# Performance work log

Hardware: AMD Instinct MI355X
Metric: run time of the kernel (lower is better)

## Reference

```python
import jax, jax.numpy as jnp
import numpy as np

LAMBDA = 0.5
TAU = 1.0
EPS = 1e-8  # torch F.cosine_similarity eps

B, D = 8192, 1024


def setup_inputs() -> dict:
    key = jax.random.key(0)
    k1, k2, k3, k4 = jax.random.split(key, 4)
    return {
        "student_query_emb": jax.random.normal(k1, (B, D), dtype=jnp.float32),
        "student_passage_emb": jax.random.normal(k2, (B, D), dtype=jnp.float32),
        "teacher_query_emb": jax.random.normal(k3, (B, D), dtype=jnp.float32),
        "teacher_passage_emb": jax.random.normal(k4, (B, D), dtype=jnp.float32),
    }


def _mse(a, b):
    d = a - b
    return jnp.mean(d * d)


def _retrieval_loss(q, p):
    # cosine sim = (q . p) / max(||q|| * ||p||, eps); normalize then matmul
    # (avoids the [B,B,D] broadcast intermediate of the torch version)
    qn = q / jnp.maximum(jnp.linalg.norm(q, axis=-1, keepdims=True), EPS)
    pn = p / jnp.maximum(jnp.linalg.norm(p, axis=-1, keepdims=True), EPS)
    logits = jnp.einsum("bd,cd->bc", qn, pn) / TAU  # [B, B]
    # cross-entropy with labels = arange(B): pick the diagonal log-prob
    logprobs = jax.nn.log_softmax(logits, axis=-1)
    return -jnp.mean(jnp.diagonal(logprobs))


def reference(student_query_emb, student_passage_emb, teacher_query_emb, teacher_passage_emb):
    distill = 0.5 * (_mse(student_query_emb, teacher_query_emb)
                     + _mse(student_passage_emb, teacher_passage_emb))
    retrieval = _retrieval_loss(student_query_emb, student_passage_emb)
    return LAMBDA * distill + (1.0 - LAMBDA) * retrieval
```

## Files before the change

kernel.cpp:

```cpp
#include <hip/hip_runtime.h>
#include <hip/hip_bf16.h>

typedef unsigned short u16;
typedef unsigned char u8;
typedef float f32x4 __attribute__((ext_vector_type(4)));
typedef int int4v __attribute__((ext_vector_type(4)));
typedef int int8v __attribute__((ext_vector_type(8)));

#define B_ROWS 8192
#define D_DIM  1024
#define FP8_SCALE 16.0f
#define ACC_UNSCALE (1.0f/256.0f)


__global__ void __launch_bounds__(256) prep_kernel(
    const float* __restrict__ sq, const float* __restrict__ sp,
    const float* __restrict__ tq, const float* __restrict__ tp,
    int* __restrict__ qn, int* __restrict__ pn,
    float* __restrict__ ppq, float* __restrict__ ppp, float* __restrict__ ppd)
{
    const int wave = threadIdx.x >> 6;
    const int l    = threadIdx.x & 63;
    const int r    = blockIdx.x * 4 + wave;
    const size_t rb4 = (size_t)r * (D_DIM / 4);

    const float4* Q4 = (const float4*)sq + rb4;
    const float4* P4 = (const float4*)sp + rb4;
    const float4* A4 = (const float4*)tq + rb4;
    const float4* B4 = (const float4*)tp + rb4;

    float4 qv[4], pv[4];
    float sq2 = 0.f, sp2 = 0.f, dq = 0.f, dp = 0.f, qp = 0.f;
    #pragma unroll
    for (int j = 0; j < 4; ++j) {
        const int idx = j * 64 + l;
        float4 q = Q4[idx], p = P4[idx], a = A4[idx], b = B4[idx];
        qv[j] = q; pv[j] = p;
        sq2 += q.x*q.x + q.y*q.y + q.z*q.z + q.w*q.w;
        sp2 += p.x*p.x + p.y*p.y + p.z*p.z + p.w*p.w;
        float dx = q.x-a.x, dy = q.y-a.y, dz = q.z-a.z, dw = q.w-a.w;
        dq += dx*dx + dy*dy + dz*dz + dw*dw;
        dx = p.x-b.x; dy = p.y-b.y; dz = p.z-b.z; dw = p.w-b.w;
        dp += dx*dx + dy*dy + dz*dz + dw*dw;
        qp += q.x*p.x + q.y*p.y + q.z*p.z + q.w*p.w;
    }

    #pragma unroll
    for (int m = 1; m <= 32; m <<= 1) {
        sq2 += __shfl_xor(sq2, m);
        sp2 += __shfl_xor(sp2, m);
        dq  += __shfl_xor(dq, m);
        dp  += __shfl_xor(dp, m);
        qp  += __shfl_xor(qp, m);
    }

    const float rq = 1.0f / fmaxf(sqrtf(sq2), 1e-8f);
    const float rp = 1.0f / fmaxf(sqrtf(sp2), 1e-8f);

    if (l == 0) {
        ppq[r] = dq;
        ppp[r] = dp;
        ppd[r] = qp * rq * rp;
    }

    const float fq = rq * FP8_SCALE;
    const float fp = rp * FP8_SCALE;
    int* qrow = qn + (size_t)r * (D_DIM / 4);
    int* prow = pn + (size_t)r * (D_DIM / 4);
    #pragma unroll
    for (int j = 0; j < 4; ++j) {
        const int idx = j * 64 + l;
        int pk = __builtin_amdgcn_cvt_pk_fp8_f32(qv[j].x * fq, qv[j].y * fq, 0, false);
        pk     = __builtin_amdgcn_cvt_pk_fp8_f32(qv[j].z * fq, qv[j].w * fq, pk, true);
        qrow[idx] = pk;
        pk = __builtin_amdgcn_cvt_pk_fp8_f32(pv[j].x * fp, pv[j].y * fp, 0, false);
        pk = __builtin_amdgcn_cvt_pk_fp8_f32(pv[j].z * fp, pv[j].w * fp, pk, true);
        prow[idx] = pk;
    }
}

union Frag { int8v v8; struct { int4v lo, hi; } h; };

__global__ void __launch_bounds__(512, 2) gemm_rowsum_kernel(
    const u8* __restrict__ Q, const u8* __restrict__ P,
    float* __restrict__ gpart)
{
    __shared__ u8 smA[2][256 * 128];
    __shared__ u8 smB[2][256 * 128];

    const int tid  = threadIdx.x;
    const int wave = tid >> 6;
    const int lane = tid & 63;
    const int wm   = wave >> 2;
    const int wn   = wave & 3;
    const int bm   = blockIdx.y;
    const int bn   = blockIdx.x;

    const int srow   = tid >> 3;
    const int schunk = (tid & 7) ^ (srow & 7);
    const u8* Ag = Q + (size_t)(bm * 256 + srow) * D_DIM + schunk * 16;
    const u8* Bg = P + (size_t)(bn * 256 + srow) * D_DIM + schunk * 16;
    const int ldsw = wave * 1024;

#define STAGE_A(b, rbase, k0)                                                  \
    __builtin_amdgcn_global_load_lds(                                          \
        (const __attribute__((address_space(1))) void*)(Ag + (size_t)(rbase) * D_DIM + (k0)), \
        (__attribute__((address_space(3))) void*)(&smA[b][(rbase) * 128] + ldsw), 16, 0, 0)
#define STAGE_B(b, rbase, k0)                                                  \
    __builtin_amdgcn_global_load_lds(                                          \
        (const __attribute__((address_space(1))) void*)(Bg + (size_t)(rbase) * D_DIM + (k0)), \
        (__attribute__((address_space(3))) void*)(&smB[b][(rbase) * 128] + ldsw), 16, 0, 0)

    const int quad = lane >> 4;
    const int rw   = lane & 15;
    const int r7   = lane & 7;
    const int off_lo = ((2 * quad) ^ r7) * 16;
    const int off_hi = ((2 * quad + 1) ^ r7) * 16;
    const int arow_base = (wm * 128 + rw) * 128;
    const int brow_base = (wn * 64  + rw) * 128;

    f32x4 acc[8][4];
    #pragma unroll
    for (int i = 0; i < 8; ++i)
        #pragma unroll
        for (int j = 0; j < 4; ++j)
            acc[i][j] = (f32x4){0.f, 0.f, 0.f, 0.f};

    STAGE_A(0, 0, 0);   STAGE_A(0, 64, 0);   STAGE_A(0, 128, 0);   STAGE_A(0, 192, 0);
    STAGE_B(0, 0, 0);   STAGE_B(0, 64, 0);   STAGE_B(0, 128, 0);   STAGE_B(0, 192, 0);
    STAGE_A(1, 0, 128); STAGE_A(1, 64, 128); STAGE_A(1, 128, 128); STAGE_A(1, 192, 128);
    STAGE_B(1, 0, 128); STAGE_B(1, 64, 128);

#define MFMA_QUAD(mih, nih)                                                    \
    _Pragma("unroll")                                                          \
    for (int mi = 0; mi < 4; ++mi)                                             \
      _Pragma("unroll")                                                        \
      for (int ni = 0; ni < 2; ++ni)                                           \
        acc[(mih)*4 + mi][(nih)*2 + ni] =                                      \
            __builtin_amdgcn_mfma_scale_f32_16x16x128_f8f6f4(                  \
                af[(mih)*4 + mi].v8, bf[(nih)*2 + ni].v8,                      \
                acc[(mih)*4 + mi][(nih)*2 + ni],                               \
                0, 0, 0, 0x7f7f7f7f, 0, 0x7f7f7f7f);

#define KSTEP(t, DO_B1, DO_T2, VMN)                                            \
  {                                                                            \
    constexpr int cur = (t) & 1;                                               \
    if (DO_B1) { STAGE_B(cur ^ 1, 128, ((t) + 1) * 128);                       \
                 STAGE_B(cur ^ 1, 192, ((t) + 1) * 128); }                     \
    asm volatile("s_waitcnt vmcnt(" #VMN ")" ::: "memory");                    \
    __builtin_amdgcn_s_barrier();                                              \
    __builtin_amdgcn_sched_barrier(0);                                         \
    Frag af[8], bf[4];                                                         \
    const u8* sA_ = &smA[cur][0];                                              \
    const u8* sB_ = &smB[cur][0];                                              \
    _Pragma("unroll")                                                          \
    for (int mi = 0; mi < 8; ++mi)                                             \
      af[mi].h.lo = *(const int4v*)(sA_ + arow_base + mi * 2048 + off_lo);     \
    _Pragma("unroll")                                                          \
    for (int ni = 0; ni < 4; ++ni)                                             \
      bf[ni].h.lo = *(const int4v*)(sB_ + brow_base + ni * 2048 + off_lo);     \
    __builtin_amdgcn_sched_barrier(0);                                         \
    _Pragma("unroll")                                                          \
    for (int mi = 0; mi < 8; ++mi)                                             \
      af[mi].h.hi = *(const int4v*)(sA_ + arow_base + mi * 2048 + off_hi);     \
    _Pragma("unroll")                                                          \
    for (int ni = 0; ni < 4; ++ni)                                             \
      bf[ni].h.hi = *(const int4v*)(sB_ + brow_base + ni * 2048 + off_hi);     \
    asm volatile("s_waitcnt lgkmcnt(0)" ::: "memory");                         \
    __builtin_amdgcn_sched_barrier(0);                                         \
    __builtin_amdgcn_s_barrier();                                              \
    __builtin_amdgcn_s_setprio(1); MFMA_QUAD(0, 0) __builtin_amdgcn_s_setprio(0); \
    if (DO_T2) { STAGE_A(cur, 0,   ((t) + 2) * 128); STAGE_A(cur, 64,  ((t) + 2) * 128); } \
    __builtin_amdgcn_s_setprio(1); MFMA_QUAD(0, 1) __builtin_amdgcn_s_setprio(0); \
    if (DO_T2) { STAGE_A(cur, 128, ((t) + 2) * 128); STAGE_A(cur, 192, ((t) + 2) * 128); } \
    __builtin_amdgcn_s_setprio(1); MFMA_QUAD(1, 0) __builtin_amdgcn_s_setprio(0); \
    if (DO_T2) { STAGE_B(cur, 0,   ((t) + 2) * 128); STAGE_B(cur, 64,  ((t) + 2) * 128); } \
    __builtin_amdgcn_s_setprio(1); MFMA_QUAD(1, 1) __builtin_amdgcn_s_setprio(0); \
  }

    KSTEP(0, true,  true,  8)
    KSTEP(1, true,  true,  8)
    KSTEP(2, true,  true,  8)
    KSTEP(3, true,  true,  8)
    KSTEP(4, true,  true,  8)
    KSTEP(5, true,  true,  8)
    KSTEP(6, true,  false, 8)
    KSTEP(7, false, false, 0)

#undef KSTEP
#undef MFMA_QUAD
#undef STAGE_A
#undef STAGE_B

    float esum[8][4];
    #pragma unroll
    for (int mi = 0; mi < 8; ++mi)
        #pragma unroll
        for (int r = 0; r < 4; ++r) {
            float s = 0.f;
            #pragma unroll
            for (int ni = 0; ni < 4; ++ni)
                s += __expf(acc[mi][ni][r] * ACC_UNSCALE);
            esum[mi][r] = s;
        }
    #pragma unroll
    for (int m = 1; m <= 8; m <<= 1)
        #pragma unroll
        for (int mi = 0; mi < 8; ++mi)
            #pragma unroll
            for (int r = 0; r < 4; ++r)
                esum[mi][r] += __shfl_xor(esum[mi][r], m);

    if (rw == 0) {
        float* dst = gpart + (size_t)(bn * 4 + wn) * B_ROWS
                   + bm * 256 + wm * 128;
        #pragma unroll
        for (int mi = 0; mi < 8; ++mi)
            #pragma unroll
            for (int r = 0; r < 4; ++r)
                dst[mi * 16 + quad * 4 + r] = esum[mi][r];
    }
}

__global__ void __launch_bounds__(256) reduce_kernel(
    const float* __restrict__ gpart,
    const float* __restrict__ ppq, const float* __restrict__ ppp,
    const float* __restrict__ ppd, float4* __restrict__ bpart)
{
    const int t = threadIdx.x;
    const int r = blockIdx.x * 256 + t;
    float s = 0.f;
    #pragma unroll 8
    for (int j = 0; j < 128; ++j) s += gpart[(size_t)j * B_ROWS + r];
    float ls = logf(s);
    float v2 = ppq[r], v3 = ppp[r], v4 = ppd[r];
    #pragma unroll
    for (int m = 1; m <= 32; m <<= 1) {
        ls += __shfl_xor(ls, m);
        v2 += __shfl_xor(v2, m);
        v3 += __shfl_xor(v3, m);
        v4 += __shfl_xor(v4, m);
    }
    __shared__ float red[4][4];
    if ((t & 63) == 0) {
        red[t >> 6][0] = ls; red[t >> 6][1] = v2;
        red[t >> 6][2] = v3; red[t >> 6][3] = v4;
    }
    __syncthreads();
    if (t == 0) {
        float4 o;
        o.x = red[0][0] + red[1][0] + red[2][0] + red[3][0];
        o.y = red[0][1] + red[1][1] + red[2][1] + red[3][1];
        o.z = red[0][2] + red[1][2] + red[2][2] + red[3][2];
        o.w = red[0][3] + red[1][3] + red[2][3] + red[3][3];
        bpart[blockIdx.x] = o;
    }
}

__global__ void __launch_bounds__(64) finalize_kernel(
    const float4* __restrict__ bpart, float* __restrict__ out)
{
    const int t = threadIdx.x;
    float4 v = (t < 32) ? bpart[t] : (float4){0.f, 0.f, 0.f, 0.f};
    #pragma unroll
    for (int m = 1; m <= 16; m <<= 1) {
        v.x += __shfl_xor(v.x, m);
        v.y += __shfl_xor(v.y, m);
        v.z += __shfl_xor(v.z, m);
        v.w += __shfl_xor(v.w, m);
    }
    if (t == 0) {
        const float inv_bd = 1.0f / ((float)B_ROWS * (float)D_DIM);
        float distill   = 0.5f * (v.y + v.z) * inv_bd;
        float retrieval = (v.x - v.w) / (float)B_ROWS;
        out[0] = 0.5f * distill + 0.5f * retrieval;
    }
}

extern "C" void kernel_launch(void* const* d_in, const int* in_sizes, int n_in,
                              void* d_out, int out_size, void* d_ws, size_t ws_size,
                              hipStream_t stream) {
    const float* sq = (const float*)d_in[0];
    const float* sp = (const float*)d_in[1];
    const float* tq = (const float*)d_in[2];
    const float* tp = (const float*)d_in[3];

    char* ws = (char*)d_ws;
    float*  ppq   = (float*)(ws);
    float*  ppp   = (float*)(ws + 32768);
    float*  ppd   = (float*)(ws + 65536);
    float4* bpart = (float4*)(ws + 98304);
    float*  gpart = (float*)(ws + 131072);
    int*    qn    = (int*)(ws + 131072 + (size_t)128 * B_ROWS * 4);
    int*    pn    = (int*)((char*)qn + (size_t)B_ROWS * D_DIM);

    prep_kernel<<<B_ROWS / 4, 256, 0, stream>>>(sq, sp, tq, tp, qn, pn, ppq, ppp, ppd);
    gemm_rowsum_kernel<<<dim3(32, 32), 512, 0, stream>>>((const u8*)qn, (const u8*)pn, gpart);
    reduce_kernel<<<32, 256, 0, stream>>>(gpart, ppq, ppp, ppd, bpart);
    finalize_kernel<<<1, 64, 0, stream>>>(bpart, (float*)d_out);
}
```

Before: 234.2 us.

## Interleave LDS fragment loads with MFMA quadrants in fp8 GEMM k-step

Splits the per-k-step LDS fragment reads into three phases, each followed by one MFMA quadrant, so shared-memory reads for later quadrants can overlap earlier matrix math. All global-to-LDS staging for step t+2 is moved to after the third quadrant, behind an extra barrier. The goal is to shorten the LDS-read stall before the first MFMA. In exchange it adds three more workgroup barriers per k-step and groups the global prefetch into one burst, which may cost more than the overlap it gains.

```diff
diff --git a/kernel.cpp b/kernel.cpp
--- a/kernel.cpp
+++ b/kernel.cpp
@@ -131,7 +131,12 @@
     STAGE_A(1, 0, 128); STAGE_A(1, 64, 128); STAGE_A(1, 128, 128); STAGE_A(1, 192, 128);
     STAGE_B(1, 0, 128); STAGE_B(1, 64, 128);
 
+#define LGKM_FENCE                                                             \
+    asm volatile("s_waitcnt lgkmcnt(0)" ::: "memory");                         \
+    __builtin_amdgcn_sched_barrier(0);
+
 #define MFMA_QUAD(mih, nih)                                                    \
+    __builtin_amdgcn_s_setprio(1);                                             \
     _Pragma("unroll")                                                          \
     for (int mi = 0; mi < 4; ++mi)                                             \
       _Pragma("unroll")                                                        \
@@ -140,42 +145,70 @@
             __builtin_amdgcn_mfma_scale_f32_16x16x128_f8f6f4(                  \
                 af[(mih)*4 + mi].v8, bf[(nih)*2 + ni].v8,                      \
                 acc[(mih)*4 + mi][(nih)*2 + ni],                               \
-                0, 0, 0, 0x7f7f7f7f, 0, 0x7f7f7f7f);
+                0, 0, 0, 0x7f7f7f7f, 0, 0x7f7f7f7f);                           \
+    __builtin_amdgcn_s_setprio(0);
 
 #define KSTEP(t, DO_B1, DO_T2, VMN)                                            \
   {                                                                            \
     constexpr int cur = (t) & 1;                                               \
+    const u8* sA_ = &smA[cur][0];                                              \
+    const u8* sB_ = &smB[cur][0];                                              \
+    Frag af[8], bf[4];                                                         \
+                  \
     if (DO_B1) { STAGE_B(cur ^ 1, 128, ((t) + 1) * 128);                       \
                  STAGE_B(cur ^ 1, 192, ((t) + 1) * 128); }                     \
     asm volatile("s_waitcnt vmcnt(" #VMN ")" ::: "memory");                    \
     __builtin_amdgcn_s_barrier();                                              \
     __builtin_amdgcn_sched_barrier(0);                                         \
-    Frag af[8], bf[4];                                                         \
-    const u8* sA_ = &smA[cur][0];                                              \
-    const u8* sB_ = &smB[cur][0];                                              \
-    _Pragma("unroll")                                                          \
-    for (int mi = 0; mi < 8; ++mi)                                             \
+                        \
+    _Pragma("unroll")                                                          \
+    for (int mi = 0; mi < 4; ++mi)                                             \
       af[mi].h.lo = *(const int4v*)(sA_ + arow_base + mi * 2048 + off_lo);     \
     _Pragma("unroll")                                                          \
-    for (int ni = 0; ni < 4; ++ni)                                             \
+    for (int ni = 0; ni < 2; ++ni)                                             \
       bf[ni].h.lo = *(const int4v*)(sB_ + brow_base + ni * 2048 + off_lo);     \
     __builtin_amdgcn_sched_barrier(0);                                         \
     _Pragma("unroll")                                                          \
-    for (int mi = 0; mi < 8; ++mi)                                             \
+    for (int mi = 0; mi < 4; ++mi)                                             \
       af[mi].h.hi = *(const int4v*)(sA_ + arow_base + mi * 2048 + off_hi);     \
     _Pragma("unroll")                                                          \
-    for (int ni = 0; ni < 4; ++ni)                                             \
+    for (int ni = 0; ni < 2; ++ni)                                             \
       bf[ni].h.hi = *(const int4v*)(sB_ + brow_base + ni * 2048 + off_hi);     \
-    asm volatile("s_waitcnt lgkmcnt(0)" ::: "memory");                         \
+    __builtin_amdgcn_s_barrier();                                              \
+    LGKM_FENCE                                                                 \
+    MFMA_QUAD(0, 0)                                                            \
+                                                         \
+    _Pragma("unroll")                                                          \
+    for (int ni = 2; ni < 4; ++ni)                                             \
+      bf[ni].h.lo = *(const int4v*)(sB_ + brow_base + ni * 2048 + off_lo);     \
+    _Pragma("unroll")                                                          \
+    for (int ni = 2; ni < 4; ++ni)                                             \
+      bf[ni].h.hi = *(const int4v*)(sB_ + brow_base + ni * 2048 + off_hi);     \
+    __builtin_amdgcn_s_barrier();                                              \
+    LGKM_FENCE                                                                 \
+    MFMA_QUAD(0, 1)                                                            \
+                                \
+    _Pragma("unroll")                                                          \
+    for (int mi = 4; mi < 8; ++mi)                                             \
+      af[mi].h.lo = *(const int4v*)(sA_ + arow_base + mi * 2048 + off_lo);     \
     __builtin_amdgcn_sched_barrier(0);                                         \
-    __builtin_amdgcn_s_barrier();                                              \
-    __builtin_amdgcn_s_setprio(1); MFMA_QUAD(0, 0) __builtin_amdgcn_s_setprio(0); \
-    if (DO_T2) { STAGE_A(cur, 0,   ((t) + 2) * 128); STAGE_A(cur, 64,  ((t) + 2) * 128); } \
-    __builtin_amdgcn_s_setprio(1); MFMA_QUAD(0, 1) __builtin_amdgcn_s_setprio(0); \
-    if (DO_T2) { STAGE_A(cur, 128, ((t) + 2) * 128); STAGE_A(cur, 192, ((t) + 2) * 128); } \
-    __builtin_amdgcn_s_setprio(1); MFMA_QUAD(1, 0) __builtin_amdgcn_s_setprio(0); \
-    if (DO_T2) { STAGE_B(cur, 0,   ((t) + 2) * 128); STAGE_B(cur, 64,  ((t) + 2) * 128); } \
-    __builtin_amdgcn_s_setprio(1); MFMA_QUAD(1, 1) __builtin_amdgcn_s_setprio(0); \
+    _Pragma("unroll")                                                          \
+    for (int mi = 4; mi < 8; ++mi)                                             \
+      af[mi].h.hi = *(const int4v*)(sA_ + arow_base + mi * 2048 + off_hi);     \
+    __builtin_amdgcn_s_barrier();                                              \
+    LGKM_FENCE                                                                 \
+    MFMA_QUAD(1, 0)                                                            \
+       \
+    __builtin_amdgcn_s_barrier();                                              \
+    __builtin_amdgcn_sched_barrier(0);                                         \
+                       \
+    if (DO_T2) { STAGE_A(cur, 0,   ((t) + 2) * 128);                           \
+                 STAGE_A(cur, 64,  ((t) + 2) * 128);                           \
+                 STAGE_A(cur, 128, ((t) + 2) * 128);                           \
+                 STAGE_A(cur, 192, ((t) + 2) * 128);                           \
+                 STAGE_B(cur, 0,   ((t) + 2) * 128);                           \
+                 STAGE_B(cur, 64,  ((t) + 2) * 128); }                         \
+    MFMA_QUAD(1, 1)                                                            \
   }
 
     KSTEP(0, true,  true,  8)
@@ -189,6 +222,7 @@
 
 #undef KSTEP
 #undef MFMA_QUAD
+#undef LGKM_FENCE
 #undef STAGE_A
 #undef STAGE_B
 
```

Result: no change. 237.3 us (+1.3%).

## Load GEMM B operand directly from global to registers and swizzle blocks per XCD

Applied to the files above, without the earlier changes.

The P (B-operand) tile is no longer staged through LDS. Each wave now loads its B fragments straight from global memory into registers at the start of every k-step, which halves shared-memory usage and removes the B staging and LDS reads. The 2D grid is also flattened to 1D with an XCD-aware mapping, so blocks on the same XCD share B column tiles for better L2 reuse. In exchange, B global-load latency is not prefetched ahead of the MFMAs, and waves with the same wn fetch identical B rows redundantly through the cache.

```diff
diff --git a/kernel.cpp b/kernel.cpp
--- a/kernel.cpp
+++ b/kernel.cpp
@@ -86,30 +86,28 @@
     float* __restrict__ gpart)
 {
     __shared__ u8 smA[2][256 * 128];
-    __shared__ u8 smB[2][256 * 128];
 
     const int tid  = threadIdx.x;
     const int wave = tid >> 6;
     const int lane = tid & 63;
     const int wm   = wave >> 2;
     const int wn   = wave & 3;
-    const int bm   = blockIdx.y;
-    const int bn   = blockIdx.x;
+
+    const int bid = blockIdx.x;
+    const int xcd = bid & 7;
+    const int idx = bid >> 3;
+    const int bn  = (xcd << 2) | (idx & 3);
+    const int bm  = idx >> 2;
 
     const int srow   = tid >> 3;
     const int schunk = (tid & 7) ^ (srow & 7);
     const u8* Ag = Q + (size_t)(bm * 256 + srow) * D_DIM + schunk * 16;
-    const u8* Bg = P + (size_t)(bn * 256 + srow) * D_DIM + schunk * 16;
     const int ldsw = wave * 1024;
 
 #define STAGE_A(b, rbase, k0)                                                  \
     __builtin_amdgcn_global_load_lds(                                          \
         (const __attribute__((address_space(1))) void*)(Ag + (size_t)(rbase) * D_DIM + (k0)), \
         (__attribute__((address_space(3))) void*)(&smA[b][(rbase) * 128] + ldsw), 16, 0, 0)
-#define STAGE_B(b, rbase, k0)                                                  \
-    __builtin_amdgcn_global_load_lds(                                          \
-        (const __attribute__((address_space(1))) void*)(Bg + (size_t)(rbase) * D_DIM + (k0)), \
-        (__attribute__((address_space(3))) void*)(&smB[b][(rbase) * 128] + ldsw), 16, 0, 0)
 
     const int quad = lane >> 4;
     const int rw   = lane & 15;
@@ -117,7 +115,8 @@
     const int off_lo = ((2 * quad) ^ r7) * 16;
     const int off_hi = ((2 * quad + 1) ^ r7) * 16;
     const int arow_base = (wm * 128 + rw) * 128;
-    const int brow_base = (wn * 64  + rw) * 128;
+
+    const u8* Bd = P + (size_t)(bn * 256 + wn * 64 + rw) * D_DIM + quad * 32;
 
     f32x4 acc[8][4];
     #pragma unroll
@@ -127,70 +126,70 @@
             acc[i][j] = (f32x4){0.f, 0.f, 0.f, 0.f};
 
     STAGE_A(0, 0, 0);   STAGE_A(0, 64, 0);   STAGE_A(0, 128, 0);   STAGE_A(0, 192, 0);
-    STAGE_B(0, 0, 0);   STAGE_B(0, 64, 0);   STAGE_B(0, 128, 0);   STAGE_B(0, 192, 0);
     STAGE_A(1, 0, 128); STAGE_A(1, 64, 128); STAGE_A(1, 128, 128); STAGE_A(1, 192, 128);
-    STAGE_B(1, 0, 128); STAGE_B(1, 64, 128);
-
-#define MFMA_QUAD(mih, nih)                                                    \
+
+#define SB0 __builtin_amdgcn_sched_barrier(0);
+
+#define MFMA_HALF(mih)                                                         \
+    __builtin_amdgcn_s_setprio(1);                                             \
     _Pragma("unroll")                                                          \
     for (int mi = 0; mi < 4; ++mi)                                             \
       _Pragma("unroll")                                                        \
-      for (int ni = 0; ni < 2; ++ni)                                           \
-        acc[(mih)*4 + mi][(nih)*2 + ni] =                                      \
+      for (int ni = 0; ni < 4; ++ni)                                           \
+        acc[(mih)*4 + mi][ni] =                                                \
             __builtin_amdgcn_mfma_scale_f32_16x16x128_f8f6f4(                  \
-                af[(mih)*4 + mi].v8, bf[(nih)*2 + ni].v8,                      \
-                acc[(mih)*4 + mi][(nih)*2 + ni],                               \
-                0, 0, 0, 0x7f7f7f7f, 0, 0x7f7f7f7f);
-
-#define KSTEP(t, DO_B1, DO_T2, VMN)                                            \
+                af[(mih)*4 + mi].v8, b[ni].v8,                                 \
+                acc[(mih)*4 + mi][ni],                                         \
+                0, 0, 0, 0x7f7f7f7f, 0, 0x7f7f7f7f);                           \
+    __builtin_amdgcn_s_setprio(0);
+
+#define KSTEP(t, DO_T2)                                                        \
   {                                                                            \
     constexpr int cur = (t) & 1;                                               \
-    if (DO_B1) { STAGE_B(cur ^ 1, 128, ((t) + 1) * 128);                       \
-                 STAGE_B(cur ^ 1, 192, ((t) + 1) * 128); }                     \
-    asm volatile("s_waitcnt vmcnt(" #VMN ")" ::: "memory");                    \
+    const u8* sA_ = &smA[cur][0];                                              \
+    Frag af[8], b[4];                                                          \
+               \
+    _Pragma("unroll")                                                          \
+    for (int ni = 0; ni < 4; ++ni) {                                           \
+      b[ni].h.lo = *(const int4v*)(Bd + ni * 16 * D_DIM + (t) * 128);          \
+      b[ni].h.hi = *(const int4v*)(Bd + ni * 16 * D_DIM + (t) * 128 + 16);     \
+    }                                                                          \
+            \
+    asm volatile("s_waitcnt vmcnt(12)" ::: "memory");                          \
     __builtin_amdgcn_s_barrier();                                              \
-    __builtin_amdgcn_sched_barrier(0);                                         \
-    Frag af[8], bf[4];                                                         \
-    const u8* sA_ = &smA[cur][0];                                              \
-    const u8* sB_ = &smB[cur][0];                                              \
+    SB0                                                                        \
+                  \
     _Pragma("unroll")                                                          \
     for (int mi = 0; mi < 8; ++mi)                                             \
       af[mi].h.lo = *(const int4v*)(sA_ + arow_base + mi * 2048 + off_lo);     \
-    _Pragma("unroll")                                                          \
-    for (int ni = 0; ni < 4; ++ni)                                             \
-      bf[ni].h.lo = *(const int4v*)(sB_ + brow_base + ni * 2048 + off_lo);     \
-    __builtin_amdgcn_sched_barrier(0);                                         \
+    SB0                                                                        \
     _Pragma("unroll")                                                          \
     for (int mi = 0; mi < 8; ++mi)                                             \
       af[mi].h.hi = *(const int4v*)(sA_ + arow_base + mi * 2048 + off_hi);     \
-    _Pragma("unroll")                                                          \
-    for (int ni = 0; ni < 4; ++ni)                                             \
-      bf[ni].h.hi = *(const int4v*)(sB_ + brow_base + ni * 2048 + off_hi);     \
     asm volatile("s_waitcnt lgkmcnt(0)" ::: "memory");                         \
-    __builtin_amdgcn_sched_barrier(0);                                         \
-    __builtin_amdgcn_s_barrier();                                              \
-    __builtin_amdgcn_s_setprio(1); MFMA_QUAD(0, 0) __builtin_amdgcn_s_setprio(0); \
-    if (DO_T2) { STAGE_A(cur, 0,   ((t) + 2) * 128); STAGE_A(cur, 64,  ((t) + 2) * 128); } \
-    __builtin_amdgcn_s_setprio(1); MFMA_QUAD(0, 1) __builtin_amdgcn_s_setprio(0); \
-    if (DO_T2) { STAGE_A(cur, 128, ((t) + 2) * 128); STAGE_A(cur, 192, ((t) + 2) * 128); } \
-    __builtin_amdgcn_s_setprio(1); MFMA_QUAD(1, 0) __builtin_amdgcn_s_setprio(0); \
-    if (DO_T2) { STAGE_B(cur, 0,   ((t) + 2) * 128); STAGE_B(cur, 64,  ((t) + 2) * 128); } \
-    __builtin_amdgcn_s_setprio(1); MFMA_QUAD(1, 1) __builtin_amdgcn_s_setprio(0); \
+    SB0                                                                        \
+    __builtin_amdgcn_s_barrier();         \
+    MFMA_HALF(0)                                                               \
+    if (DO_T2) { STAGE_A(cur, 0,   ((t) + 2) * 128);                           \
+                 STAGE_A(cur, 64,  ((t) + 2) * 128);                           \
+                 STAGE_A(cur, 128, ((t) + 2) * 128);                           \
+                 STAGE_A(cur, 192, ((t) + 2) * 128); }                         \
+    MFMA_HALF(1)                                                               \
   }
 
-    KSTEP(0, true,  true,  8)
-    KSTEP(1, true,  true,  8)
-    KSTEP(2, true,  true,  8)
-    KSTEP(3, true,  true,  8)
-    KSTEP(4, true,  true,  8)
-    KSTEP(5, true,  true,  8)
-    KSTEP(6, true,  false, 8)
-    KSTEP(7, false, false, 0)
+    KSTEP(0, true)
+    KSTEP(1, true)
+    KSTEP(2, true)
+    KSTEP(3, true)
+    KSTEP(4, true)
+    KSTEP(5, true)
+    KSTEP(6, false)
+    KSTEP(7, false)
 
 #undef KSTEP
-#undef MFMA_QUAD
+#undef MFMA_HALF
+#undef SB0
 #undef STAGE_A
-#undef STAGE_B
 
     float esum[8][4];
     #pragma unroll
@@ -295,7 +294,7 @@
     int*    pn    = (int*)((char*)qn + (size_t)B_ROWS * D_DIM);
 
     prep_kernel<<<B_ROWS / 4, 256, 0, stream>>>(sq, sp, tq, tp, qn, pn, ppq, ppp, ppd);
-    gemm_rowsum_kernel<<<dim3(32, 32), 512, 0, stream>>>((const u8*)qn, (const u8*)pn, gpart);
+    gemm_rowsum_kernel<<<1024, 512, 0, stream>>>((const u8*)qn, (const u8*)pn, gpart);
     reduce_kernel<<<32, 256, 0, stream>>>(gpart, ppq, ppp, ppd, bpart);
     finalize_kernel<<<1, 64, 0, stream>>>(bpart, (float*)d_out);
 }
```

Result: slower. 247.6 us (+5.7%).

## Interleave LDS fragment reads with MFMAs using staged lgkmcnt waits

Applied to the files above, without the earlier changes.

Reorders each K-step so LDS fragment loads for A and B are issued in groups, with partial lgkmcnt waits, and MFMAs that already have their operands start while later fragments are still arriving. Previously every LDS read had to finish before any MFMA ran. All global prefetch stages for step t+2 now issue together after the second barrier instead of being spread between MFMA quads. The aim is to hide LDS read latency behind matrix math. In exchange, global-load issue is bunched together, and the hand-counted lgkmcnt values must match the actual number of outstanding LDS ops or correctness breaks.

```diff
diff --git a/kernel.cpp b/kernel.cpp
--- a/kernel.cpp
+++ b/kernel.cpp
@@ -131,51 +131,68 @@
     STAGE_A(1, 0, 128); STAGE_A(1, 64, 128); STAGE_A(1, 128, 128); STAGE_A(1, 192, 128);
     STAGE_B(1, 0, 128); STAGE_B(1, 64, 128);
 
-#define MFMA_QUAD(mih, nih)                                                    \
-    _Pragma("unroll")                                                          \
-    for (int mi = 0; mi < 4; ++mi)                                             \
-      _Pragma("unroll")                                                        \
-      for (int ni = 0; ni < 2; ++ni)                                           \
-        acc[(mih)*4 + mi][(nih)*2 + ni] =                                      \
-            __builtin_amdgcn_mfma_scale_f32_16x16x128_f8f6f4(                  \
-                af[(mih)*4 + mi].v8, bf[(nih)*2 + ni].v8,                      \
-                acc[(mih)*4 + mi][(nih)*2 + ni],                               \
-                0, 0, 0, 0x7f7f7f7f, 0, 0x7f7f7f7f);
+#define SB0 __builtin_amdgcn_sched_barrier(0);
+#define WAITL(n) asm volatile("s_waitcnt lgkmcnt(" #n ")" ::: "memory"); SB0
+
+#define READ_AF(mi)                                                            \
+    af[mi].h.lo = *(const int4v*)(sA_ + arow_base + (mi) * 2048 + off_lo);     \
+    af[mi].h.hi = *(const int4v*)(sA_ + arow_base + (mi) * 2048 + off_hi);
+#define READ_BF(ni)                                                            \
+    bf[ni].h.lo = *(const int4v*)(sB_ + brow_base + (ni) * 2048 + off_lo);     \
+    bf[ni].h.hi = *(const int4v*)(sB_ + brow_base + (ni) * 2048 + off_hi);
+
+#define MFMA1(mi, ni)                                                          \
+    acc[mi][ni] = __builtin_amdgcn_mfma_scale_f32_16x16x128_f8f6f4(            \
+        af[mi].v8, bf[ni].v8, acc[mi][ni],                                     \
+        0, 0, 0, 0x7f7f7f7f, 0, 0x7f7f7f7f);
 
 #define KSTEP(t, DO_B1, DO_T2, VMN)                                            \
   {                                                                            \
     constexpr int cur = (t) & 1;                                               \
+    const u8* sA_ = &smA[cur][0];                                              \
+    const u8* sB_ = &smB[cur][0];                                              \
+    Frag af[8], bf[4];                                                         \
+                  \
     if (DO_B1) { STAGE_B(cur ^ 1, 128, ((t) + 1) * 128);                       \
                  STAGE_B(cur ^ 1, 192, ((t) + 1) * 128); }                     \
     asm volatile("s_waitcnt vmcnt(" #VMN ")" ::: "memory");                    \
     __builtin_amdgcn_s_barrier();                                              \
-    __builtin_amdgcn_sched_barrier(0);                                         \
-    Frag af[8], bf[4];                                                         \
-    const u8* sA_ = &smA[cur][0];                                              \
-    const u8* sB_ = &smB[cur][0];                                              \
-    _Pragma("unroll")                                                          \
-    for (int mi = 0; mi < 8; ++mi)                                             \
-      af[mi].h.lo = *(const int4v*)(sA_ + arow_base + mi * 2048 + off_lo);     \
-    _Pragma("unroll")                                                          \
-    for (int ni = 0; ni < 4; ++ni)                                             \
-      bf[ni].h.lo = *(const int4v*)(sB_ + brow_base + ni * 2048 + off_lo);     \
-    __builtin_amdgcn_sched_barrier(0);                                         \
-    _Pragma("unroll")                                                          \
-    for (int mi = 0; mi < 8; ++mi)                                             \
-      af[mi].h.hi = *(const int4v*)(sA_ + arow_base + mi * 2048 + off_hi);     \
-    _Pragma("unroll")                                                          \
-    for (int ni = 0; ni < 4; ++ni)                                             \
-      bf[ni].h.hi = *(const int4v*)(sB_ + brow_base + ni * 2048 + off_hi);     \
-    asm volatile("s_waitcnt lgkmcnt(0)" ::: "memory");                         \
-    __builtin_amdgcn_sched_barrier(0);                                         \
+    SB0                                                                        \
+                                             \
+    READ_BF(0) READ_BF(1) READ_AF(0)                                           \
+    READ_AF(1) READ_AF(2) READ_AF(3)                                           \
+    WAITL(6)                                         \
+    __builtin_amdgcn_s_setprio(1);                                             \
+    MFMA1(0, 0) MFMA1(0, 1)                                                    \
+    __builtin_amdgcn_s_setprio(0);                                             \
+    READ_BF(2) READ_BF(3) READ_AF(4)                                           \
+    WAITL(6)                                         \
+    __builtin_amdgcn_s_setprio(1);                                             \
+    MFMA1(1, 0) MFMA1(1, 1) MFMA1(2, 0) MFMA1(2, 1) MFMA1(3, 0) MFMA1(3, 1)    \
+    __builtin_amdgcn_s_setprio(0);                                             \
+    READ_AF(5) READ_AF(6) READ_AF(7)                                           \
+    WAITL(6)                                             \
+    __builtin_amdgcn_s_setprio(1);                                             \
+    MFMA1(0, 2) MFMA1(0, 3) MFMA1(1, 2) MFMA1(1, 3)                            \
+    MFMA1(2, 2) MFMA1(2, 3) MFMA1(3, 2) MFMA1(3, 3)                            \
+    MFMA1(4, 0) MFMA1(4, 1)                                                    \
+    __builtin_amdgcn_s_setprio(0);                                             \
+    WAITL(0)             \
     __builtin_amdgcn_s_barrier();                                              \
-    __builtin_amdgcn_s_setprio(1); MFMA_QUAD(0, 0) __builtin_amdgcn_s_setprio(0); \
-    if (DO_T2) { STAGE_A(cur, 0,   ((t) + 2) * 128); STAGE_A(cur, 64,  ((t) + 2) * 128); } \
-    __builtin_amdgcn_s_setprio(1); MFMA_QUAD(0, 1) __builtin_amdgcn_s_setprio(0); \
-    if (DO_T2) { STAGE_A(cur, 128, ((t) + 2) * 128); STAGE_A(cur, 192, ((t) + 2) * 128); } \
-    __builtin_amdgcn_s_setprio(1); MFMA_QUAD(1, 0) __builtin_amdgcn_s_setprio(0); \
-    if (DO_T2) { STAGE_B(cur, 0,   ((t) + 2) * 128); STAGE_B(cur, 64,  ((t) + 2) * 128); } \
-    __builtin_amdgcn_s_setprio(1); MFMA_QUAD(1, 1) __builtin_amdgcn_s_setprio(0); \
+    SB0                                                                        \
+                    \
+    if (DO_T2) { STAGE_A(cur, 0,   ((t) + 2) * 128);                           \
+                 STAGE_A(cur, 64,  ((t) + 2) * 128);                           \
+                 STAGE_A(cur, 128, ((t) + 2) * 128);                           \
+                 STAGE_A(cur, 192, ((t) + 2) * 128);                           \
+                 STAGE_B(cur, 0,   ((t) + 2) * 128);                           \
+                 STAGE_B(cur, 64,  ((t) + 2) * 128); }                         \
+    __builtin_amdgcn_s_setprio(1);                                             \
+    MFMA1(4, 2) MFMA1(4, 3)                                                    \
+    MFMA1(5, 0) MFMA1(5, 1) MFMA1(5, 2) MFMA1(5, 3)                            \
+    MFMA1(6, 0) MFMA1(6, 1) MFMA1(6, 2) MFMA1(6, 3)                            \
+    MFMA1(7, 0) MFMA1(7, 1) MFMA1(7, 2) MFMA1(7, 3)                            \
+    __builtin_amdgcn_s_setprio(0);                                             \
   }
 
     KSTEP(0, true,  true,  8)
@@ -188,7 +205,11 @@
     KSTEP(7, false, false, 0)
 
 #undef KSTEP
-#undef MFMA_QUAD
+#undef MFMA1
+#undef READ_AF
+#undef READ_BF
+#undef WAITL
+#undef SB0
 #undef STAGE_A
 #undef STAGE_B
 
```

Result: no change. 231.6 us (-1.1%).
